# Optimization experiments

Hardware: AMD Instinct MI355X
Metric: run time of the kernel (lower is better)

The kernel has to match this reference:

```python
import jax, jax.numpy as jnp
import numpy as np

# SNNConfig constants (see init_kwargs)
TAU_MEM = 0.02
TAU_SYN = 0.005
DT = 0.001
THRESHOLD = 1.0
BETA = 10.0  # fast-sigmoid surrogate beta

BATCH, TIME, IN_DIM, HIDDEN = 32, 1024, 512, 512


@jax.custom_vjp
def spike_fn(v):
    """Heaviside spike with fast-sigmoid surrogate gradient."""
    return (v > THRESHOLD).astype(v.dtype)


def _spike_fwd(v):
    return spike_fn(v), v


def _spike_bwd(v, g):
    x = v - THRESHOLD
    surr = 1.0 / jnp.square(1.0 + BETA * jnp.abs(x))
    return (g * surr,)


spike_fn.defvjp(_spike_fwd, _spike_bwd)


def setup_inputs() -> dict:
    key = jax.random.key(0)
    k1, k2 = jax.random.split(key)
    spikes = jax.random.uniform(k1, (BATCH, TIME, IN_DIM), dtype=jnp.float32)
    # xavier_uniform for (IN_DIM, HIDDEN)
    limit = np.sqrt(6.0 / (IN_DIM + HIDDEN))
    W = jax.random.uniform(k2, (IN_DIM, HIDDEN), dtype=jnp.float32,
                           minval=-limit, maxval=limit)
    b = jnp.zeros((HIDDEN,), dtype=jnp.float32)
    return {"spikes": spikes, "W": W, "b": b}


def reference(spikes, W, b):
    # spikes: [B, T, I]; W: [I, H]; b: [H]
    alpha_mem = jnp.exp(jnp.asarray(-DT / TAU_MEM, dtype=spikes.dtype))
    alpha_syn = jnp.exp(jnp.asarray(-DT / TAU_SYN, dtype=spikes.dtype))
    # hoist the per-step GEMM into one big contraction: [B, T, H]
    I_in = jnp.einsum('bti,ih->bth', spikes, W) + b

    B, T, H = I_in.shape
    v0 = jnp.zeros((B, H), dtype=spikes.dtype)
    s0 = jnp.zeros((B, H), dtype=spikes.dtype)

    def lif_step(carry, i_t):
        v_mem, i_syn = carry
        i_syn = alpha_syn * i_syn + i_t
        v_mem = alpha_mem * v_mem + i_syn
        out = spike_fn(v_mem)
        v_mem = v_mem - out * THRESHOLD  # soft reset
        return (v_mem, i_syn), out

    _, out_spikes = jax.lax.scan(lif_step, (v0, s0), I_in.transpose(1, 0, 2))
    return out_spikes.transpose(1, 0, 2)  # [B, T, H]
```

## Files before the change

### kernel.cpp

```cpp
#include <hip/hip_runtime.h>
#include <hip/hip_bf16.h>

constexpr int BATCH  = 32;
constexpr int TIME   = 1024;
constexpr int IN_DIM = 512;
constexpr int HIDDEN = 512;

constexpr int GM = BATCH * TIME;
constexpr int GN = HIDDEN;
constexpr int GK = IN_DIM;

#define WAITCNT_LGKMCNT(n) (0xF | (0x7 << 4) | (((n) & 0xF) << 8) | (0x3 << 14))
#define COMPILER_FENCE() asm volatile("" ::: "memory")

constexpr int BM = 128;
constexpr int BN = 128;
constexpr int BK = 16;
constexpr int LDAs = BM + 4;
constexpr int LDBs = BN + 4;

__global__ __launch_bounds__(256) void sgemm_bias_kernel(
    const float* __restrict__ A,
    const float* __restrict__ B,
    const float* __restrict__ bias,
    float* __restrict__ C)
{
    __shared__ __align__(16) float As[BK * LDAs];
    __shared__ __align__(16) float Bs[BK * LDBs];

    const int tid = threadIdx.x;
    const int bm  = blockIdx.x * BM;
    const int bn  = blockIdx.y * BN;

    const int w    = tid >> 6;
    const int lane = tid & 63;
    const int row0 = (w >> 1) * 64 + (lane >> 3) * 8;
    const int col0 = (w & 1)  * 64 + (lane & 7)  * 8;

    const int ar0 = tid >> 2;
    const int ac  = (tid & 3) << 2;
    const int br0 = tid >> 5;
    const int bc  = (tid & 31) << 2;

    float acc[8][8];
    #pragma unroll
    for (int i = 0; i < 8; ++i)
        #pragma unroll
        for (int j = 0; j < 8; ++j) acc[i][j] = 0.0f;

    #pragma unroll 1
    for (int k0 = 0; k0 < GK; k0 += BK) {
        float4 va0 = *reinterpret_cast<const float4*>(A + (size_t)(bm + ar0) * GK + k0 + ac);
        float4 va1 = *reinterpret_cast<const float4*>(A + (size_t)(bm + ar0 + 64) * GK + k0 + ac);
        float4 vb0 = *reinterpret_cast<const float4*>(B + (size_t)(k0 + br0) * GN + bn + bc);
        float4 vb1 = *reinterpret_cast<const float4*>(B + (size_t)(k0 + br0 + 8) * GN + bn + bc);

        __syncthreads();

        As[(ac + 0) * LDAs + ar0] = va0.x;
        As[(ac + 1) * LDAs + ar0] = va0.y;
        As[(ac + 2) * LDAs + ar0] = va0.z;
        As[(ac + 3) * LDAs + ar0] = va0.w;
        As[(ac + 0) * LDAs + ar0 + 64] = va1.x;
        As[(ac + 1) * LDAs + ar0 + 64] = va1.y;
        As[(ac + 2) * LDAs + ar0 + 64] = va1.z;
        As[(ac + 3) * LDAs + ar0 + 64] = va1.w;
        *reinterpret_cast<float4*>(&Bs[br0 * LDBs + bc]) = vb0;
        *reinterpret_cast<float4*>(&Bs[(br0 + 8) * LDBs + bc]) = vb1;

        __syncthreads();

        #pragma unroll
        for (int kk = 0; kk < BK; ++kk) {
            const float4 a0 = *reinterpret_cast<const float4*>(&As[kk * LDAs + row0]);
            const float4 a1 = *reinterpret_cast<const float4*>(&As[kk * LDAs + row0 + 4]);
            const float4 b0 = *reinterpret_cast<const float4*>(&Bs[kk * LDBs + col0]);
            const float4 b1 = *reinterpret_cast<const float4*>(&Bs[kk * LDBs + col0 + 4]);
            const float arr[8] = {a0.x, a0.y, a0.z, a0.w, a1.x, a1.y, a1.z, a1.w};
            const float brr[8] = {b0.x, b0.y, b0.z, b0.w, b1.x, b1.y, b1.z, b1.w};
            #pragma unroll
            for (int i = 0; i < 8; ++i)
                #pragma unroll
                for (int j = 0; j < 8; ++j)
                    acc[i][j] = fmaf(arr[i], brr[j], acc[i][j]);
        }
    }

    #pragma unroll
    for (int i = 0; i < 8; ++i) {
        const size_t r = (size_t)(bm + row0 + i);
        #pragma unroll
        for (int j = 0; j < 8; j += 4) {
            float4 v;
            v.x = __fadd_rn(acc[i][j + 0], bias[bn + col0 + j + 0]);
            v.y = __fadd_rn(acc[i][j + 1], bias[bn + col0 + j + 1]);
            v.z = __fadd_rn(acc[i][j + 2], bias[bn + col0 + j + 2]);
            v.w = __fadd_rn(acc[i][j + 3], bias[bn + col0 + j + 3]);
            *reinterpret_cast<float4*>(&C[r * GN + bn + col0 + j]) = v;
        }
    }
}

constexpr int SH   = 64;
constexpr int SCH  = 16;
constexpr int NCHK = TIME / SCH;
constexpr int RT   = 256;
constexpr int RCH  = RT / SCH;

__global__ __launch_bounds__(256) void lif_scan_kernel(
    const float* __restrict__ I,
    float* __restrict__ O)
{
    __shared__ __align__(16) float ring[RT * SH];
    __shared__ int prod_f[3];
    __shared__ int cons_c;

    const int blk  = blockIdx.x;
    const int b    = blk >> 3;
    const int h0   = (blk & 7) * SH;
    const int wave = threadIdx.x >> 6;
    const int lane = threadIdx.x & 63;
    const size_t base0 = (size_t)b * TIME * HIDDEN + h0;

    if (threadIdx.x < 3) prod_f[threadIdx.x] = -1;
    if (threadIdx.x == 3) cons_c = 0;
    __syncthreads();

    if (wave < 3) {
        const int p = wave;
        const float* g0 = I + base0 + (size_t)(lane >> 4) * HIDDEN + (lane & 15) * 4;

        float4 rr[2][4];
        auto loadc = [&](float4* r, int c) {
            #pragma unroll
            for (int u = 0; u < 4; ++u)
                r[u] = *reinterpret_cast<const float4*>(
                    g0 + (size_t)(c * SCH + u * 4) * HIDDEN);
        };

        loadc(rr[0], p);
        int q = 0;
        #pragma unroll 1
        for (int c = p; c < NCHK; c += 3) {
            const int cn = c + 3;
            loadc(rr[q ^ 1], (cn < NCHK) ? cn : c);
            if (c >= RCH) {
                while (__hip_atomic_load(&cons_c, __ATOMIC_RELAXED,
                                         __HIP_MEMORY_SCOPE_WORKGROUP)
                       < c - RCH + 1) { }
                COMPILER_FENCE();
            }
            const int slot = (c & (RCH - 1)) * SCH;
            float* dst = &ring[(slot + (lane >> 4)) * SH + (lane & 15) * 4];
            #pragma unroll
            for (int u = 0; u < 4; ++u)
                *reinterpret_cast<float4*>(dst + u * 4 * SH) = rr[q][u];
            COMPILER_FENCE();
            __builtin_amdgcn_s_waitcnt(WAITCNT_LGKMCNT(0));
            COMPILER_FENCE();
            __hip_atomic_store(&prod_f[p], c, __ATOMIC_RELAXED,
                               __HIP_MEMORY_SCOPE_WORKGROUP);
            q ^= 1;
        }
    } else {
        const float am = 0.95122942450071400910f;
        const float as = 0.81873075307798185867f;
        float v = 0.0f, s = 0.0f;
        float* o0 = O + base0 + lane;

        #pragma unroll 1
        for (int c = 0; c < NCHK; ++c) {
            const int src = c % 3;
            while (__hip_atomic_load(&prod_f[src], __ATOMIC_RELAXED,
                                     __HIP_MEMORY_SCOPE_WORKGROUP) < c) { }
            COMPILER_FENCE();
            const int slot = (c & (RCH - 1)) * SCH;
            float ob[SCH];
            #pragma unroll
            for (int u = 0; u < SCH; ++u) {
                const float x = ring[(slot + u) * SH + lane];
                s = __fadd_rn(__fmul_rn(as, s), x);
                v = __fadd_rn(__fmul_rn(am, v), s);
                const float o = (v > 1.0f) ? 1.0f : 0.0f;
                v = __fsub_rn(v, o);
                ob[u] = o;
            }
            COMPILER_FENCE();
            __hip_atomic_store(&cons_c, c + 1, __ATOMIC_RELAXED,
                               __HIP_MEMORY_SCOPE_WORKGROUP);
            #pragma unroll
            for (int u = 0; u < SCH; ++u)
                o0[(size_t)(c * SCH + u) * HIDDEN] = ob[u];
        }
    }
}

extern "C" void kernel_launch(void* const* d_in, const int* in_sizes, int n_in,
                              void* d_out, int out_size, void* d_ws, size_t ws_size,
                              hipStream_t stream) {
    const float* spikes = (const float*)d_in[0];
    const float* W      = (const float*)d_in[1];
    const float* bias   = (const float*)d_in[2];
    float* out  = (float*)d_out;
    float* I_in = (float*)d_ws;

    dim3 g1(GM / BM, GN / BN);
    sgemm_bias_kernel<<<g1, 256, 0, stream>>>(spikes, W, bias, I_in);

    lif_scan_kernel<<<BATCH * HIDDEN / SH, 256, 0, stream>>>(I_in, out);
}
```

Before: 313.4 us.

## Replace LDS ring-buffer producer waves with cache-prefetch helper waves in LIF scan

Removes the shared-memory ring buffer and producer/consumer handshake from the LIF scan. Three helper waves now only touch upcoming chunks of the input (summing them into a discarded register) to pull them into cache, staying at most a fixed number of chunks ahead of the compute wave. The compute wave then loads its 32-step chunk straight from global memory, which should now hit in cache. This cuts LDS traffic and per-chunk synchronisation, at the cost of depending on cache residency and issuing redundant global reads.

```diff
diff --git a/kernel.cpp b/kernel.cpp
--- a/kernel.cpp
+++ b/kernel.cpp
@@ -9,9 +9,6 @@
 constexpr int GM = BATCH * TIME;
 constexpr int GN = HIDDEN;
 constexpr int GK = IN_DIM;
-
-#define WAITCNT_LGKMCNT(n) (0xF | (0x7 << 4) | (((n) & 0xF) << 8) | (0x3 << 14))
-#define COMPILER_FENCE() asm volatile("" ::: "memory")
 
 constexpr int BM = 128;
 constexpr int BN = 128;
@@ -101,96 +98,72 @@
     }
 }
 
-constexpr int SH   = 64;
-constexpr int SCH  = 16;
-constexpr int NCHK = TIME / SCH;
-constexpr int RT   = 256;
-constexpr int RCH  = RT / SCH;
+constexpr int CCH   = 32;
+constexpr int CNCH  = TIME / CCH;
+constexpr int AHEAD = 12;
 
 __global__ __launch_bounds__(256) void lif_scan_kernel(
     const float* __restrict__ I,
     float* __restrict__ O)
 {
-    __shared__ __align__(16) float ring[RT * SH];
-    __shared__ int prod_f[3];
-    __shared__ int cons_c;
+    __shared__ int progress;
 
     const int blk  = blockIdx.x;
     const int b    = blk >> 3;
-    const int h0   = (blk & 7) * SH;
+    const int h0   = (blk & 7) * 64;
     const int wave = threadIdx.x >> 6;
     const int lane = threadIdx.x & 63;
-    const size_t base0 = (size_t)b * TIME * HIDDEN + h0;
+    const size_t base = (size_t)b * TIME * HIDDEN + h0 + lane;
 
-    if (threadIdx.x < 3) prod_f[threadIdx.x] = -1;
-    if (threadIdx.x == 3) cons_c = 0;
+    if (threadIdx.x == 0) progress = 0;
     __syncthreads();
 
     if (wave < 3) {
-        const int p = wave;
-        const float* g0 = I + base0 + (size_t)(lane >> 4) * HIDDEN + (lane & 15) * 4;
-
-        float4 rr[2][4];
-        auto loadc = [&](float4* r, int c) {
+        const float* g0 = I + base;
+        float acc = 0.0f;
+        #pragma unroll 1
+        for (int c = wave; c < CNCH; c += 3) {
+            while (__hip_atomic_load(&progress, __ATOMIC_RELAXED,
+                                     __HIP_MEMORY_SCOPE_WORKGROUP) + AHEAD < c) { }
+            const float* gp = g0 + (size_t)c * CCH * HIDDEN;
+            float a0 = 0.f, a1 = 0.f, a2 = 0.f, a3 = 0.f;
             #pragma unroll
-            for (int u = 0; u < 4; ++u)
-                r[u] = *reinterpret_cast<const float4*>(
-                    g0 + (size_t)(c * SCH + u * 4) * HIDDEN);
-        };
-
-        loadc(rr[0], p);
-        int q = 0;
-        #pragma unroll 1
-        for (int c = p; c < NCHK; c += 3) {
-            const int cn = c + 3;
-            loadc(rr[q ^ 1], (cn < NCHK) ? cn : c);
-            if (c >= RCH) {
-                while (__hip_atomic_load(&cons_c, __ATOMIC_RELAXED,
-                                         __HIP_MEMORY_SCOPE_WORKGROUP)
-                       < c - RCH + 1) { }
-                COMPILER_FENCE();
+            for (int u = 0; u < CCH; u += 4) {
+                a0 += gp[(size_t)(u + 0) * HIDDEN];
+                a1 += gp[(size_t)(u + 1) * HIDDEN];
+                a2 += gp[(size_t)(u + 2) * HIDDEN];
+                a3 += gp[(size_t)(u + 3) * HIDDEN];
             }
-            const int slot = (c & (RCH - 1)) * SCH;
-            float* dst = &ring[(slot + (lane >> 4)) * SH + (lane & 15) * 4];
-            #pragma unroll
-            for (int u = 0; u < 4; ++u)
-                *reinterpret_cast<float4*>(dst + u * 4 * SH) = rr[q][u];
-            COMPILER_FENCE();
-            __builtin_amdgcn_s_waitcnt(WAITCNT_LGKMCNT(0));
-            COMPILER_FENCE();
-            __hip_atomic_store(&prod_f[p], c, __ATOMIC_RELAXED,
-                               __HIP_MEMORY_SCOPE_WORKGROUP);
-            q ^= 1;
+            acc += (a0 + a1) + (a2 + a3);
         }
+        asm volatile("" :: "v"(acc));
     } else {
         const float am = 0.95122942450071400910f;
         const float as = 0.81873075307798185867f;
         float v = 0.0f, s = 0.0f;
-        float* o0 = O + base0 + lane;
+        const float* Ip = I + base;
+        float*       Op = O + base;
 
         #pragma unroll 1
-        for (int c = 0; c < NCHK; ++c) {
-            const int src = c % 3;
-            while (__hip_atomic_load(&prod_f[src], __ATOMIC_RELAXED,
-                                     __HIP_MEMORY_SCOPE_WORKGROUP) < c) { }
-            COMPILER_FENCE();
-            const int slot = (c & (RCH - 1)) * SCH;
-            float ob[SCH];
+        for (int c = 0; c < CNCH; ++c) {
+            float buf[CCH];
             #pragma unroll
-            for (int u = 0; u < SCH; ++u) {
-                const float x = ring[(slot + u) * SH + lane];
-                s = __fadd_rn(__fmul_rn(as, s), x);
+            for (int u = 0; u < CCH; ++u)
+                buf[u] = Ip[(size_t)(c * CCH + u) * HIDDEN];
+            __hip_atomic_store(&progress, c, __ATOMIC_RELAXED,
+                               __HIP_MEMORY_SCOPE_WORKGROUP);
+            float ob[CCH];
+            #pragma unroll
+            for (int u = 0; u < CCH; ++u) {
+                s = __fadd_rn(__fmul_rn(as, s), buf[u]);
                 v = __fadd_rn(__fmul_rn(am, v), s);
                 const float o = (v > 1.0f) ? 1.0f : 0.0f;
                 v = __fsub_rn(v, o);
                 ob[u] = o;
             }
-            COMPILER_FENCE();
-            __hip_atomic_store(&cons_c, c + 1, __ATOMIC_RELAXED,
-                               __HIP_MEMORY_SCOPE_WORKGROUP);
             #pragma unroll
-            for (int u = 0; u < SCH; ++u)
-                o0[(size_t)(c * SCH + u) * HIDDEN] = ob[u];
+            for (int u = 0; u < CCH; ++u)
+                Op[(size_t)(c * CCH + u) * HIDDEN] = ob[u];
         }
     }
 }
@@ -207,5 +180,5 @@
     dim3 g1(GM / BM, GN / BN);
     sgemm_bias_kernel<<<g1, 256, 0, stream>>>(spikes, W, bias, I_in);
 
-    lif_scan_kernel<<<BATCH * HIDDEN / SH, 256, 0, stream>>>(I_in, out);
+    lif_scan_kernel<<<256, 256, 0, stream>>>(I_in, out);
 }
```

New measurement: 317.9 us. About the same (+1.4%).
